# Kernel tuning notes

Hardware: AMD Instinct MI355X
Metric: run time of the kernel (lower is better)

## Reference

```python
import jax, jax.numpy as jnp
import numpy as np


def setup_inputs() -> dict:
    key = jax.random.key(0)
    k = jax.random.split(key, 6)
    B, N, Cin, Cd, nE = 64, 197, 768, 256, 8192
    return {
        "z": jax.random.normal(k[0], (B, N, Cin), dtype=jnp.float32),
        "emb": jax.random.truncated_normal(k[1], -3.0, 3.0, (nE, Cd), dtype=jnp.float32),
        "W_compress": jax.random.normal(k[2], (Cin, Cd), dtype=jnp.float32) * 0.02,
        "b_compress": jnp.zeros((Cd,), dtype=jnp.float32),
        "W_expand": jax.random.normal(k[3], (Cd, Cin), dtype=jnp.float32) * 0.02,
        "b_expand": jnp.zeros((Cin,), dtype=jnp.float32),
    }


def reference(z, emb, W_compress, b_compress, W_expand, b_expand):
    # compress: [B,N,Cin] -> [B,N,Cd]
    zc = jnp.einsum('bnc,cd->bnd', z, W_compress) + b_compress
    zf = zc.reshape(-1, zc.shape[-1])  # [M, Cd]
    # squared distances to codebook: ||z||^2 + ||e||^2 - 2 z.e  -> [M, nE]
    d = (jnp.sum(zf * zf, axis=1, keepdims=True)
         + jnp.sum(emb * emb, axis=1)
         - 2.0 * (zf @ emb.T))
    indices = jnp.argmin(d, axis=1)  # [M]
    z_q = emb[indices]               # gather [M, Cd]
    sg = jax.lax.stop_gradient
    # training-mode commitment/codebook loss
    loss = jnp.mean((sg(z_q) - zf) ** 2) + 2.0 * jnp.mean((z_q - sg(zf)) ** 2)
    # straight-through estimator
    z_q = sg(z_q) + zf - sg(zf)
    z_q = z_q.reshape(zc.shape)
    out = jnp.einsum('bnd,dc->bnc', z_q, W_expand) + b_expand  # [B,N,Cin]
    return (out, loss)
```

## Files before the change

### kernel.cpp

```cpp
#include <hip/hip_runtime.h>
#include <stdint.h>

#define M_TOK 12608
#define MPAD  12672
#define CIN   768
#define CD    256
#define NE    8192
#define NCHUNK 8
#define CHUNK  1024

typedef unsigned long long u64;
typedef unsigned int u32;
typedef _Float16 f16;
typedef _Float16 f16x8 __attribute__((ext_vector_type(8)));
typedef _Float16 f16x4 __attribute__((ext_vector_type(4)));
typedef float f32x4 __attribute__((ext_vector_type(4)));

#if __has_builtin(__builtin_amdgcn_global_load_lds)
#define HAVE_GLL 1
#else
#define HAVE_GLL 0
#endif

__device__ __forceinline__ void stage16(const f16* src, char* lds_base, int lane)
{
#if HAVE_GLL
    __builtin_amdgcn_global_load_lds(
        (__attribute__((address_space(1))) void*)(src),
        (__attribute__((address_space(3))) void*)(lds_base), 16, 0, 0);
#else
    *(f16x8*)(lds_base + lane * 16) = *(const f16x8*)src;
#endif
}

__global__ __launch_bounds__(256) void k_enorm(const float* __restrict__ emb,
                                               float* __restrict__ enorm,
                                               f16* __restrict__ embf16,
                                               float* __restrict__ loss_slot)
{
    if (blockIdx.x == 0 && threadIdx.x == 0) *loss_slot = 0.0f;
    int row  = blockIdx.x * 4 + (threadIdx.x >> 6);
    int lane = threadIdx.x & 63;
    float4 v = *(const float4*)&emb[(size_t)row * CD + lane * 4];
    f16x4 hv = { (f16)v.x, (f16)v.y, (f16)v.z, (f16)v.w };
    *(f16x4*)&embf16[(size_t)row * CD + lane * 4] = hv;
    float s = v.x*v.x + v.y*v.y + v.z*v.z + v.w*v.w;
    #pragma unroll
    for (int o = 32; o; o >>= 1) s += __shfl_down(s, o, 64);
    if (lane == 0) enorm[row] = s;
}

__global__ __launch_bounds__(256) void k_prep_w(const float* __restrict__ Wc,
                                                const float* __restrict__ We,
                                                f16* __restrict__ wchi,
                                                f16* __restrict__ wclo,
                                                f16* __restrict__ wet)
{
    int tid = blockIdx.x * 256 + threadIdx.x;
    {
        int n = tid & 255, k = tid >> 8;
        float v = Wc[(size_t)k * CD + n];
        f16 h = (f16)v;
        wchi[(size_t)n * CIN + k] = h;
        wclo[(size_t)n * CIN + k] = (f16)(v - (float)h);
    }
    {
        int d = tid / CIN, c = tid - d * CIN;
        wet[(size_t)c * CD + d] = (f16)We[(size_t)d * CIN + c];
    }
}

__global__ __launch_bounds__(256) void k_prep_z(const float* __restrict__ z,
                                                f16* __restrict__ zhi,
                                                f16* __restrict__ zlo)
{
    size_t i4 = (size_t)blockIdx.x * 256 + threadIdx.x;
    float4 v = ((const float4*)z)[i4];
    f16x4 h = { (f16)v.x, (f16)v.y, (f16)v.z, (f16)v.w };
    f16x4 lo = { (f16)(v.x - (float)h.x), (f16)(v.y - (float)h.y),
                 (f16)(v.z - (float)h.z), (f16)(v.w - (float)h.w) };
    ((f16x4*)zhi)[i4] = h;
    ((f16x4*)zlo)[i4] = lo;
}

__global__ __launch_bounds__(256) void k_init_zc(const float* __restrict__ bc,
                                                 float* __restrict__ zc)
{
    size_t i4 = (size_t)blockIdx.x * 256 + threadIdx.x;
    ((float4*)zc)[i4] = ((const float4*)bc)[i4 & 63];
}

__global__ __launch_bounds__(256) void k_zcfin(const float* __restrict__ zc,
                                               f16* __restrict__ zcf16)
{
    size_t i4 = (size_t)blockIdx.x * 256 + threadIdx.x;
    float4 v = ((const float4*)zc)[i4];
    f16x4 h = { (f16)v.x, (f16)v.y, (f16)v.z, (f16)v.w };
    ((f16x4*)zcf16)[i4] = h;
}

__global__ __launch_bounds__(256) void k_compress3(const f16* __restrict__ zhi,
                                                   const f16* __restrict__ zlo,
                                                   const f16* __restrict__ wchi,
                                                   const f16* __restrict__ wclo,
                                                   float* __restrict__ zc)
{
    __shared__ __align__(16) f16 As[128 * 64];
    __shared__ __align__(16) f16 Bs[128 * 64];

    const int t = threadIdx.x;
    const int w = t >> 6, l = t & 63;
    const int wrow = (w >> 1) * 64, wcol = (w & 1) * 64;
    const int m0   = blockIdx.x * 128;
    const int col0 = blockIdx.y * 128;
    const int term = blockIdx.z;

    const f16* A = (term < 2)  ? zhi  : zlo;
    const f16* B = (term == 1) ? wclo : wchi;

    const int cg   = (t & 7) ^ ((t >> 3) & 7);
    const int rloc = t >> 3;
    const f16* asrc[4]; const f16* bsrc[4];
    #pragma unroll
    for (int i = 0; i < 4; ++i) {
        int r = i * 32 + rloc;
        int am = m0 + r; am = am < M_TOK ? am : (M_TOK - 1);
        asrc[i] = A + (size_t)am * CIN + cg * 8;
        bsrc[i] = B + (size_t)(col0 + r) * CIN + cg * 8;
    }
    const int prd0 = (l >> 4) ^ (l & 7);
    const int prd1 = (4 + (l >> 4)) ^ (l & 7);

    f32x4 acc[4][4];
    #pragma unroll
    for (int a = 0; a < 4; ++a)
        #pragma unroll
        for (int b = 0; b < 4; ++b) acc[a][b] = (f32x4){0.f,0.f,0.f,0.f};

    for (int ks = 0; ks < CIN / 64; ++ks) {
        __syncthreads();
        #pragma unroll
        for (int i = 0; i < 4; ++i) {
            stage16(asrc[i] + ks * 64, (char*)As + (i * 256 + w * 64) * 16, l);
            stage16(bsrc[i] + ks * 64, (char*)Bs + (i * 256 + w * 64) * 16, l);
        }
        __syncthreads();
        #pragma unroll
        for (int kk = 0; kk < 2; ++kk) {
            const int pofs = (kk ? prd1 : prd0) * 16;
            f16x8 af[4], bf[4];
            #pragma unroll
            for (int tm = 0; tm < 4; ++tm)
                af[tm] = *(const f16x8*)((const char*)As + (wrow + tm*16 + (l & 15)) * 128 + pofs);
            #pragma unroll
            for (int tn = 0; tn < 4; ++tn)
                bf[tn] = *(const f16x8*)((const char*)Bs + (wcol + tn*16 + (l & 15)) * 128 + pofs);
            #pragma unroll
            for (int tm = 0; tm < 4; ++tm)
                #pragma unroll
                for (int tn = 0; tn < 4; ++tn)
                    acc[tm][tn] = __builtin_amdgcn_mfma_f32_16x16x32_f16(af[tm], bf[tn], acc[tm][tn], 0, 0, 0);
        }
    }

    #pragma unroll
    for (int tm = 0; tm < 4; ++tm) {
        #pragma unroll
        for (int reg = 0; reg < 4; ++reg) {
            int row = m0 + wrow + tm * 16 + (l >> 4) * 4 + reg;
            if (row < M_TOK) {
                #pragma unroll
                for (int tn = 0; tn < 4; ++tn) {
                    int col = col0 + wcol + tn * 16 + (l & 15);
                    unsafeAtomicAdd(&zc[(size_t)row * CD + col], acc[tm][tn][reg]);
                }
            }
        }
    }
}

__global__ __launch_bounds__(256) void k_dist_mfma(const f16* __restrict__ zcf16,
                                                   const f16* __restrict__ embf16,
                                                   const float* __restrict__ enorm,
                                                   u64* __restrict__ part)
{
    __shared__ __align__(16) f16 As[128 * 64];
    __shared__ __align__(16) f16 Bs[128 * 64];
    __shared__ u64 wred[128][2][2];

    const int t = threadIdx.x;
    const int w = t >> 6, l = t & 63;
    const int wrow = (w >> 1) * 64, wcol = (w & 1) * 64;
    const int m0    = blockIdx.x * 128;
    const int chunk = blockIdx.y;

    const int cg   = (t & 7) ^ ((t >> 3) & 7);
    const int rloc = t >> 3;
    const f16* asrc[4]; const f16* bsrc[4];
    #pragma unroll
    for (int i = 0; i < 4; ++i) {
        int r = i * 32 + rloc;
        int am = m0 + r; am = am < M_TOK ? am : (M_TOK - 1);
        asrc[i] = zcf16 + (size_t)am * CD + cg * 8;
        bsrc[i] = embf16 + (size_t)r * CD + cg * 8;
    }
    const int prd0 = (l >> 4) ^ (l & 7);
    const int prd1 = (4 + (l >> 4)) ^ (l & 7);

    float bd[16];
    int   bcol[16];
    #pragma unroll
    for (int s = 0; s < 16; ++s) { bd[s] = __builtin_inff(); bcol[s] = 0; }

    for (int tile = 0; tile < 8; ++tile) {
        const int j0 = chunk * CHUNK + tile * 128;
        f32x4 acc[4][4];
        #pragma unroll
        for (int a = 0; a < 4; ++a)
            #pragma unroll
            for (int b = 0; b < 4; ++b) acc[a][b] = (f32x4){0.f,0.f,0.f,0.f};

        for (int ks = 0; ks < 4; ++ks) {
            __syncthreads();
            #pragma unroll
            for (int i = 0; i < 4; ++i) {
                stage16(asrc[i] + ks * 64, (char*)As + (i * 256 + w * 64) * 16, l);
                stage16(bsrc[i] + (size_t)j0 * CD + ks * 64, (char*)Bs + (i * 256 + w * 64) * 16, l);
            }
            __syncthreads();
            #pragma unroll
            for (int kk = 0; kk < 2; ++kk) {
                const int pofs = (kk ? prd1 : prd0) * 16;
                f16x8 af[4], bf[4];
                #pragma unroll
                for (int tm = 0; tm < 4; ++tm)
                    af[tm] = *(const f16x8*)((const char*)As + (wrow + tm*16 + (l & 15)) * 128 + pofs);
                #pragma unroll
                for (int tn = 0; tn < 4; ++tn)
                    bf[tn] = *(const f16x8*)((const char*)Bs + (wcol + tn*16 + (l & 15)) * 128 + pofs);
                #pragma unroll
                for (int tm = 0; tm < 4; ++tm)
                    #pragma unroll
                    for (int tn = 0; tn < 4; ++tn)
                        acc[tm][tn] = __builtin_amdgcn_mfma_f32_16x16x32_f16(af[tm], bf[tn], acc[tm][tn], 0, 0, 0);
            }
        }

        const int cb = j0 + wcol + (l & 15);
        float en0 = enorm[cb], en1 = enorm[cb + 16], en2 = enorm[cb + 32], en3 = enorm[cb + 48];
        #pragma unroll
        for (int tm = 0; tm < 4; ++tm) {
            #pragma unroll
            for (int reg = 0; reg < 4; ++reg) {
                const int s = tm * 4 + reg;
                float d0 = fmaf(acc[tm][0][reg], -2.f, en0);
                float d1 = fmaf(acc[tm][1][reg], -2.f, en1);
                float d2 = fmaf(acc[tm][2][reg], -2.f, en2);
                float d3 = fmaf(acc[tm][3][reg], -2.f, en3);
                float da = d1 < d0 ? d1 : d0;  int ca = d1 < d0 ? cb + 16 : cb;
                float db = d3 < d2 ? d3 : d2;  int cc = d3 < d2 ? cb + 48 : cb + 32;
                float dm = db < da ? db : da;  int cm = db < da ? cc : ca;
                if (dm < bd[s]) { bd[s] = dm; bcol[s] = cm; }
            }
        }
    }

    #pragma unroll
    for (int tm = 0; tm < 4; ++tm) {
        #pragma unroll
        for (int reg = 0; reg < 4; ++reg) {
            const int s = tm * 4 + reg;
            u32 u = __float_as_uint(bd[s]);
            u = (u & 0x80000000u) ? ~u : (u | 0x80000000u);
            u64 b  = ((u64)u << 32) | (u32)bcol[s];
            u64 sc = ~0ull;
            #pragma unroll
            for (int off = 1; off <= 8; off <<= 1) {
                u64 ob = __shfl_xor(b, off, 64);
                u64 os = __shfl_xor(sc, off, 64);
                u64 nb = b < ob ? b : ob;
                u64 mx = b < ob ? ob : b;
                sc = sc < os ? sc : os;
                sc = sc < mx ? sc : mx;
                b = nb;
            }
            if ((l & 15) == 0) {
                int row = wrow + tm * 16 + (l >> 4) * 4 + reg;
                wred[row][w & 1][0] = b;
                wred[row][w & 1][1] = sc;
            }
        }
    }
    __syncthreads();
    if (t < 128) {
        u64 b0 = wred[t][0][0], s0 = wred[t][0][1];
        u64 b1 = wred[t][1][0], s1 = wred[t][1][1];
        u64 B  = b0 < b1 ? b0 : b1;
        u64 mx = b0 < b1 ? b1 : b0;
        u64 S  = s0 < s1 ? s0 : s1;
        S = S < mx ? S : mx;
        int row = m0 + t;
        if (row < M_TOK) {
            part[((size_t)row * NCHUNK + chunk) * 2 + 0] = B;
            part[((size_t)row * NCHUNK + chunk) * 2 + 1] = S;
        }
    }
}

__global__ __launch_bounds__(256) void k_rescore(const float* __restrict__ zc,
                                                 const float* __restrict__ emb,
                                                 const float* __restrict__ enorm,
                                                 const u64* __restrict__ part,
                                                 int* __restrict__ idxp,
                                                 float* __restrict__ loss_slot)
{
    const int row = blockIdx.x * 4 + (threadIdx.x >> 6);
    const int l   = threadIdx.x & 63;
    __shared__ float lsum[4];

    float4 zr = *(const float4*)&zc[(size_t)row * CD + l * 4];
    u64 best = ~0ull;
    for (int c = 0; c < 16; ++c) {
        u64 key = part[(size_t)row * 16 + c];
        int col = (int)((u32)key & (NE - 1));
        float4 er = *(const float4*)&emb[(size_t)col * CD + l * 4];
        float p = zr.x*er.x + zr.y*er.y + zr.z*er.z + zr.w*er.w;
        #pragma unroll
        for (int o = 32; o; o >>= 1) p += __shfl_xor(p, o, 64);
        float d = fmaf(p, -2.f, enorm[col]);
        u32 u = __float_as_uint(d);
        u = (u & 0x80000000u) ? ~u : (u | 0x80000000u);
        u64 k2 = ((u64)u << 32) | (u32)col;
        best = k2 < best ? k2 : best;
    }
    float zn = zr.x*zr.x + zr.y*zr.y + zr.z*zr.z + zr.w*zr.w;
    #pragma unroll
    for (int o = 32; o; o >>= 1) zn += __shfl_xor(zn, o, 64);

    u32 hi = (u32)(best >> 32);
    float dbest = (hi & 0x80000000u) ? __uint_as_float(hi & 0x7fffffffu)
                                     : __uint_as_float(~hi);
    if (l == 0) {
        idxp[row] = (int)((u32)best & (NE - 1));
        lsum[threadIdx.x >> 6] = dbest + zn;
    }
    __syncthreads();
    if (threadIdx.x == 0) {
        float tot = lsum[0] + lsum[1] + lsum[2] + lsum[3];
        atomicAdd(loss_slot, tot * (3.0f / 3227648.0f));
    }
}

__global__ __launch_bounds__(256) void k_expand_mfma(const f16* __restrict__ embf16,
                                                     const int* __restrict__ idxp,
                                                     const f16* __restrict__ wet,
                                                     const float* __restrict__ be,
                                                     float* __restrict__ out)
{
    __shared__ __align__(16) f16 As[128 * 64];
    __shared__ __align__(16) f16 Bs[128 * 64];

    const int t = threadIdx.x;
    const int w = t >> 6, l = t & 63;
    const int wrow = (w >> 1) * 64, wcol = (w & 1) * 64;
    const int m0   = blockIdx.x * 128;
    const int col0 = blockIdx.y * 128;

    const int cg   = (t & 7) ^ ((t >> 3) & 7);
    const int rloc = t >> 3;
    const f16* asrc[4]; const f16* bsrc[4];
    #pragma unroll
    for (int i = 0; i < 4; ++i) {
        int r = i * 32 + rloc;
        int m = m0 + r; m = m < M_TOK ? m : (M_TOK - 1);
        int er = idxp[m];
        asrc[i] = embf16 + (size_t)er * CD + cg * 8;
        bsrc[i] = wet + (size_t)(col0 + r) * CD + cg * 8;
    }
    const int prd0 = (l >> 4) ^ (l & 7);
    const int prd1 = (4 + (l >> 4)) ^ (l & 7);

    f32x4 acc[4][4];
    #pragma unroll
    for (int a = 0; a < 4; ++a)
        #pragma unroll
        for (int b = 0; b < 4; ++b) acc[a][b] = (f32x4){0.f,0.f,0.f,0.f};

    for (int ks = 0; ks < 4; ++ks) {
        __syncthreads();
        #pragma unroll
        for (int i = 0; i < 4; ++i) {
            stage16(asrc[i] + ks * 64, (char*)As + (i * 256 + w * 64) * 16, l);
            stage16(bsrc[i] + ks * 64, (char*)Bs + (i * 256 + w * 64) * 16, l);
        }
        __syncthreads();
        #pragma unroll
        for (int kk = 0; kk < 2; ++kk) {
            const int pofs = (kk ? prd1 : prd0) * 16;
            f16x8 af[4], bf[4];
            #pragma unroll
            for (int tm = 0; tm < 4; ++tm)
                af[tm] = *(const f16x8*)((const char*)As + (wrow + tm*16 + (l & 15)) * 128 + pofs);
            #pragma unroll
            for (int tn = 0; tn < 4; ++tn)
                bf[tn] = *(const f16x8*)((const char*)Bs + (wcol + tn*16 + (l & 15)) * 128 + pofs);
            #pragma unroll
            for (int tm = 0; tm < 4; ++tm)
                #pragma unroll
                for (int tn = 0; tn < 4; ++tn)
                    acc[tm][tn] = __builtin_amdgcn_mfma_f32_16x16x32_f16(af[tm], bf[tn], acc[tm][tn], 0, 0, 0);
        }
    }

    float bev[4];
    #pragma unroll
    for (int tn = 0; tn < 4; ++tn) bev[tn] = be[col0 + wcol + tn * 16 + (l & 15)];
    #pragma unroll
    for (int tm = 0; tm < 4; ++tm) {
        #pragma unroll
        for (int reg = 0; reg < 4; ++reg) {
            int row = m0 + wrow + tm * 16 + (l >> 4) * 4 + reg;
            if (row < M_TOK) {
                #pragma unroll
                for (int tn = 0; tn < 4; ++tn) {
                    int col = col0 + wcol + tn * 16 + (l & 15);
                    out[(size_t)row * CIN + col] = acc[tm][tn][reg] + bev[tn];
                }
            }
        }
    }
}

#define BK1 16
__global__ __launch_bounds__(256) void k_compress(const float* __restrict__ z,
                                                  const float* __restrict__ W,
                                                  const float* __restrict__ bias,
                                                  float* __restrict__ zc,
                                                  f16* __restrict__ zcf16)
{
    __shared__ __align__(16) float As[BK1][64 + 4];
    __shared__ __align__(16) float Bs[BK1][64 + 4];
    const int t  = threadIdx.x;
    const int tx = t & 15, ty = t >> 4;
    const int row0 = blockIdx.x * 64;
    const int col0 = blockIdx.y * 64;

    const int la_r = t >> 2;
    const int la_k = (t & 3) << 2;
    const int lb_k = t >> 4;
    const int lb_n = (t & 15) << 2;

    float acc[4][4] = {};

    for (int k0 = 0; k0 < CIN; k0 += BK1) {
        float4 a4 = *(const float4*)&z[(size_t)(row0 + la_r) * CIN + k0 + la_k];
        float4 b4 = *(const float4*)&W[(size_t)(k0 + lb_k) * CD + col0 + lb_n];
        __syncthreads();
        As[la_k + 0][la_r] = a4.x; As[la_k + 1][la_r] = a4.y;
        As[la_k + 2][la_r] = a4.z; As[la_k + 3][la_r] = a4.w;
        *(float4*)&Bs[lb_k][lb_n] = b4;
        __syncthreads();
        #pragma unroll
        for (int k = 0; k < BK1; ++k) {
            float a[4], b[4];
            *(float4*)&a[0] = *(const float4*)&As[k][ty * 4];
            *(float4*)&b[0] = *(const float4*)&Bs[k][tx * 4];
            #pragma unroll
            for (int i = 0; i < 4; ++i)
                #pragma unroll
                for (int j = 0; j < 4; ++j)
                    acc[i][j] = fmaf(a[i], b[j], acc[i][j]);
        }
    }

    float4 bb = *(const float4*)&bias[col0 + tx * 4];
    #pragma unroll
    for (int i = 0; i < 4; ++i) {
        float4 v;
        v.x = acc[i][0] + bb.x; v.y = acc[i][1] + bb.y;
        v.z = acc[i][2] + bb.z; v.w = acc[i][3] + bb.w;
        size_t off = (size_t)(row0 + ty * 4 + i) * CD + col0 + tx * 4;
        *(float4*)&zc[off] = v;
        f16x4 hv = { (f16)v.x, (f16)v.y, (f16)v.z, (f16)v.w };
        *(f16x4*)&zcf16[off] = hv;
    }
}

extern "C" void kernel_launch(void* const* d_in, const int* in_sizes, int n_in,
                              void* d_out, int out_size, void* d_ws, size_t ws_size,
                              hipStream_t stream)
{
    (void)in_sizes; (void)n_in; (void)out_size;

    const float* z   = (const float*)d_in[0];
    const float* emb = (const float*)d_in[1];
    const float* Wc  = (const float*)d_in[2];
    const float* bc  = (const float*)d_in[3];
    const float* We  = (const float*)d_in[4];
    const float* be  = (const float*)d_in[5];

    float* out       = (float*)d_out;
    float* loss_slot = out + (size_t)M_TOK * CIN;

    char* base = (char*)d_ws;
    size_t off = 0;
    auto align_up = [](size_t x) { return (x + 255) & ~(size_t)255; };

    float* enorm = (float*)(base + off); off = align_up(off + (size_t)NE * 4);
    u64*   part  = (u64*)(base + off);   off = align_up(off + (size_t)M_TOK * 16 * 8);
    int*   idxp  = (int*)(base + off);   off = align_up(off + (size_t)M_TOK * 4);
    f16*   embf16= (f16*)(base + off);   off = align_up(off + (size_t)NE * CD * 2);
    f16*   zcf16 = (f16*)(base + off);   off = align_up(off + (size_t)MPAD * CD * 2);
    f16*   wet   = (f16*)(base + off);   off = align_up(off + (size_t)CIN * CD * 2);
    f16*   wchi  = (f16*)(base + off);   off = align_up(off + (size_t)CD * CIN * 2);
    f16*   wclo  = (f16*)(base + off);   off = align_up(off + (size_t)CD * CIN * 2);

    const size_t zsplit_bytes = (size_t)M_TOK * CIN * 2;
    bool have_split = (ws_size >= off + 2 * zsplit_bytes);
    f16 *zhi = nullptr, *zlo = nullptr;
    if (have_split) {
        zhi = (f16*)(base + off); off = align_up(off + zsplit_bytes);
        zlo = (f16*)(base + off); off = align_up(off + zsplit_bytes);
    }
    const size_t zc_bytes = (size_t)M_TOK * CD * 4;
    float* zc = (ws_size >= off + zc_bytes) ? (float*)(base + off) : out;

    k_enorm <<<NE / 4, 256, 0, stream>>>(emb, enorm, embf16, loss_slot);
    k_prep_w<<<(CIN * CD) / 256, 256, 0, stream>>>(Wc, We, wchi, wclo, wet);

    if (have_split) {
        k_prep_z  <<<((size_t)M_TOK * CIN / 4) / 256, 256, 0, stream>>>(z, zhi, zlo);
        k_init_zc <<<((size_t)M_TOK * CD / 4) / 256, 256, 0, stream>>>(bc, zc);
        k_compress3<<<dim3(MPAD / 128, CD / 128, 3), 256, 0, stream>>>(zhi, zlo, wchi, wclo, zc);
        k_zcfin   <<<((size_t)M_TOK * CD / 4) / 256, 256, 0, stream>>>(zc, zcf16);
    } else {
        k_compress<<<dim3(M_TOK / 64, CD / 64), 256, 0, stream>>>(z, Wc, bc, zc, zcf16);
    }

    k_dist_mfma  <<<dim3(MPAD / 128, NCHUNK), 256, 0, stream>>>(zcf16, embf16, enorm, part);
    k_rescore    <<<M_TOK / 4, 256, 0, stream>>>(zc, emb, enorm, part, idxp, loss_slot);
    k_expand_mfma<<<dim3(MPAD / 128, CIN / 128), 256, 0, stream>>>(embf16, idxp, wet, be, out);
}
```

Measured before the change: 315.9 us.

## Fuse prep kernels, fuse split-f16 compress terms with bias, widen distance tiles

Merges the emb-norm, weight-prep and z-split kernels into one launch with block-range dispatch. The compress GEMM now computes all three hi/lo product terms inside one block and writes zc plus its f16 copy with the bias added directly. This removes the atomic adds, the zc init kernel and the finalize kernel. The distance kernel now processes 256 codebook columns per tile with 4x8 accumulators per wave and launch_bounds(256,2). That cuts A-tile restaging but raises register and LDS pressure.

```diff
diff --git a/kernel.cpp b/kernel.cpp
--- a/kernel.cpp
+++ b/kernel.cpp
@@ -33,234 +33,242 @@
 #endif
 }
 
-__global__ __launch_bounds__(256) void k_enorm(const float* __restrict__ emb,
-                                               float* __restrict__ enorm,
-                                               f16* __restrict__ embf16,
-                                               float* __restrict__ loss_slot)
-{
-    if (blockIdx.x == 0 && threadIdx.x == 0) *loss_slot = 0.0f;
-    int row  = blockIdx.x * 4 + (threadIdx.x >> 6);
-    int lane = threadIdx.x & 63;
-    float4 v = *(const float4*)&emb[(size_t)row * CD + lane * 4];
-    f16x4 hv = { (f16)v.x, (f16)v.y, (f16)v.z, (f16)v.w };
-    *(f16x4*)&embf16[(size_t)row * CD + lane * 4] = hv;
-    float s = v.x*v.x + v.y*v.y + v.z*v.z + v.w*v.w;
-    #pragma unroll
-    for (int o = 32; o; o >>= 1) s += __shfl_down(s, o, 64);
-    if (lane == 0) enorm[row] = s;
-}
-
-__global__ __launch_bounds__(256) void k_prep_w(const float* __restrict__ Wc,
-                                                const float* __restrict__ We,
-                                                f16* __restrict__ wchi,
-                                                f16* __restrict__ wclo,
-                                                f16* __restrict__ wet)
-{
-    int tid = blockIdx.x * 256 + threadIdx.x;
-    {
-        int n = tid & 255, k = tid >> 8;
-        float v = Wc[(size_t)k * CD + n];
-        f16 h = (f16)v;
-        wchi[(size_t)n * CIN + k] = h;
-        wclo[(size_t)n * CIN + k] = (f16)(v - (float)h);
-    }
-    {
-        int d = tid / CIN, c = tid - d * CIN;
-        wet[(size_t)c * CD + d] = (f16)We[(size_t)d * CIN + c];
-    }
-}
-
-__global__ __launch_bounds__(256) void k_prep_z(const float* __restrict__ z,
-                                                f16* __restrict__ zhi,
-                                                f16* __restrict__ zlo)
-{
-    size_t i4 = (size_t)blockIdx.x * 256 + threadIdx.x;
-    float4 v = ((const float4*)z)[i4];
-    f16x4 h = { (f16)v.x, (f16)v.y, (f16)v.z, (f16)v.w };
-    f16x4 lo = { (f16)(v.x - (float)h.x), (f16)(v.y - (float)h.y),
-                 (f16)(v.z - (float)h.z), (f16)(v.w - (float)h.w) };
-    ((f16x4*)zhi)[i4] = h;
-    ((f16x4*)zlo)[i4] = lo;
-}
-
-__global__ __launch_bounds__(256) void k_init_zc(const float* __restrict__ bc,
-                                                 float* __restrict__ zc)
-{
-    size_t i4 = (size_t)blockIdx.x * 256 + threadIdx.x;
-    ((float4*)zc)[i4] = ((const float4*)bc)[i4 & 63];
-}
-
-__global__ __launch_bounds__(256) void k_zcfin(const float* __restrict__ zc,
-                                               f16* __restrict__ zcf16)
-{
-    size_t i4 = (size_t)blockIdx.x * 256 + threadIdx.x;
-    float4 v = ((const float4*)zc)[i4];
-    f16x4 h = { (f16)v.x, (f16)v.y, (f16)v.z, (f16)v.w };
-    ((f16x4*)zcf16)[i4] = h;
-}
-
-__global__ __launch_bounds__(256) void k_compress3(const f16* __restrict__ zhi,
-                                                   const f16* __restrict__ zlo,
-                                                   const f16* __restrict__ wchi,
-                                                   const f16* __restrict__ wclo,
-                                                   float* __restrict__ zc)
-{
-    __shared__ __align__(16) f16 As[128 * 64];
-    __shared__ __align__(16) f16 Bs[128 * 64];
+__global__ __launch_bounds__(256) void k_prep(const float* __restrict__ emb,
+                                              const float* __restrict__ Wc,
+                                              const float* __restrict__ We,
+                                              const float* __restrict__ z,
+                                              float* __restrict__ enorm,
+                                              f16* __restrict__ embf16,
+                                              f16* __restrict__ wchi,
+                                              f16* __restrict__ wclo,
+                                              f16* __restrict__ wet,
+                                              f16* __restrict__ zhi,
+                                              f16* __restrict__ zlo,
+                                              float* __restrict__ loss_slot)
+{
+    const int b = blockIdx.x;
+    const int t = threadIdx.x;
+    if (b < 2048) {
+        if (b == 0 && t == 0) *loss_slot = 0.0f;
+        int row  = b * 4 + (t >> 6);
+        int lane = t & 63;
+        float4 v = *(const float4*)&emb[(size_t)row * CD + lane * 4];
+        f16x4 hv = { (f16)v.x, (f16)v.y, (f16)v.z, (f16)v.w };
+        *(f16x4*)&embf16[(size_t)row * CD + lane * 4] = hv;
+        float s = v.x*v.x + v.y*v.y + v.z*v.z + v.w*v.w;
+        #pragma unroll
+        for (int o = 32; o; o >>= 1) s += __shfl_down(s, o, 64);
+        if (lane == 0) enorm[row] = s;
+    } else if (b < 2048 + 768) {
+        int tid = (b - 2048) * 256 + t;
+        {
+            int n = tid & 255, k = tid >> 8;
+            float v = Wc[(size_t)k * CD + n];
+            f16 h = (f16)v;
+            wchi[(size_t)n * CIN + k] = h;
+            wclo[(size_t)n * CIN + k] = (f16)(v - (float)h);
+        }
+        {
+            int d = tid / CIN, c = tid - d * CIN;
+            wet[(size_t)c * CD + d] = (f16)We[(size_t)d * CIN + c];
+        }
+    } else {
+        size_t i4 = (size_t)(b - 2816) * 256 + t;
+        float4 v = ((const float4*)z)[i4];
+        f16x4 h = { (f16)v.x, (f16)v.y, (f16)v.z, (f16)v.w };
+        f16x4 lo = { (f16)(v.x - (float)h.x), (f16)(v.y - (float)h.y),
+                     (f16)(v.z - (float)h.z), (f16)(v.w - (float)h.w) };
+        ((f16x4*)zhi)[i4] = h;
+        ((f16x4*)zlo)[i4] = lo;
+    }
+}
+
+__global__ __launch_bounds__(256) void k_compress_f(const f16* __restrict__ zhi,
+                                                    const f16* __restrict__ zlo,
+                                                    const f16* __restrict__ wchi,
+                                                    const f16* __restrict__ wclo,
+                                                    const float* __restrict__ bc,
+                                                    float* __restrict__ zc,
+                                                    f16* __restrict__ zcf16)
+{
+    __shared__ __align__(16) f16 Ah[128 * 64];
+    __shared__ __align__(16) f16 Al[128 * 64];
+    __shared__ __align__(16) f16 Bh[64 * 64];
+    __shared__ __align__(16) f16 Bl[64 * 64];
 
     const int t = threadIdx.x;
     const int w = t >> 6, l = t & 63;
-    const int wrow = (w >> 1) * 64, wcol = (w & 1) * 64;
+    const int wrow = w * 32;
     const int m0   = blockIdx.x * 128;
-    const int col0 = blockIdx.y * 128;
-    const int term = blockIdx.z;
-
-    const f16* A = (term < 2)  ? zhi  : zlo;
-    const f16* B = (term == 1) ? wclo : wchi;
+    const int col0 = blockIdx.y * 64;
 
     const int cg   = (t & 7) ^ ((t >> 3) & 7);
     const int rloc = t >> 3;
-    const f16* asrc[4]; const f16* bsrc[4];
+    const f16* ahsrc[4]; const f16* alsrc[4];
     #pragma unroll
     for (int i = 0; i < 4; ++i) {
-        int r = i * 32 + rloc;
-        int am = m0 + r; am = am < M_TOK ? am : (M_TOK - 1);
-        asrc[i] = A + (size_t)am * CIN + cg * 8;
-        bsrc[i] = B + (size_t)(col0 + r) * CIN + cg * 8;
-    }
-    const int prd0 = (l >> 4) ^ (l & 7);
-    const int prd1 = (4 + (l >> 4)) ^ (l & 7);
-
-    f32x4 acc[4][4];
-    #pragma unroll
-    for (int a = 0; a < 4; ++a)
-        #pragma unroll
-        for (int b = 0; b < 4; ++b) acc[a][b] = (f32x4){0.f,0.f,0.f,0.f};
+        int am = m0 + i * 32 + rloc; am = am < M_TOK ? am : (M_TOK - 1);
+        ahsrc[i] = zhi + (size_t)am * CIN + cg * 8;
+        alsrc[i] = zlo + (size_t)am * CIN + cg * 8;
+    }
+    const f16* bhsrc[2]; const f16* blsrc[2];
+    #pragma unroll
+    for (int i = 0; i < 2; ++i) {
+        int br = col0 + i * 32 + rloc;
+        bhsrc[i] = wchi + (size_t)br * CIN + cg * 8;
+        blsrc[i] = wclo + (size_t)br * CIN + cg * 8;
+    }
+
+    f32x4 acc[2][4];
+    #pragma unroll
+    for (int a = 0; a < 2; ++a)
+        #pragma unroll
+        for (int b2 = 0; b2 < 4; ++b2) acc[a][b2] = (f32x4){0.f,0.f,0.f,0.f};
 
     for (int ks = 0; ks < CIN / 64; ++ks) {
         __syncthreads();
         #pragma unroll
         for (int i = 0; i < 4; ++i) {
-            stage16(asrc[i] + ks * 64, (char*)As + (i * 256 + w * 64) * 16, l);
-            stage16(bsrc[i] + ks * 64, (char*)Bs + (i * 256 + w * 64) * 16, l);
+            stage16(ahsrc[i] + ks * 64, (char*)Ah + (i * 256 + w * 64) * 16, l);
+            stage16(alsrc[i] + ks * 64, (char*)Al + (i * 256 + w * 64) * 16, l);
+        }
+        #pragma unroll
+        for (int i = 0; i < 2; ++i) {
+            stage16(bhsrc[i] + ks * 64, (char*)Bh + (i * 256 + w * 64) * 16, l);
+            stage16(blsrc[i] + ks * 64, (char*)Bl + (i * 256 + w * 64) * 16, l);
         }
         __syncthreads();
         #pragma unroll
         for (int kk = 0; kk < 2; ++kk) {
-            const int pofs = (kk ? prd1 : prd0) * 16;
-            f16x8 af[4], bf[4];
-            #pragma unroll
-            for (int tm = 0; tm < 4; ++tm)
-                af[tm] = *(const f16x8*)((const char*)As + (wrow + tm*16 + (l & 15)) * 128 + pofs);
-            #pragma unroll
-            for (int tn = 0; tn < 4; ++tn)
-                bf[tn] = *(const f16x8*)((const char*)Bs + (wcol + tn*16 + (l & 15)) * 128 + pofs);
-            #pragma unroll
-            for (int tm = 0; tm < 4; ++tm)
-                #pragma unroll
-                for (int tn = 0; tn < 4; ++tn)
-                    acc[tm][tn] = __builtin_amdgcn_mfma_f32_16x16x32_f16(af[tm], bf[tn], acc[tm][tn], 0, 0, 0);
-        }
-    }
-
-    #pragma unroll
-    for (int tm = 0; tm < 4; ++tm) {
+            const int pofs = ((kk * 4 + (l >> 4)) ^ (l & 7)) * 16;
+            f16x8 ah[2], al[2], bh[4], bl[4];
+            #pragma unroll
+            for (int tm = 0; tm < 2; ++tm) {
+                ah[tm] = *(const f16x8*)((const char*)Ah + (wrow + tm*16 + (l & 15)) * 128 + pofs);
+                al[tm] = *(const f16x8*)((const char*)Al + (wrow + tm*16 + (l & 15)) * 128 + pofs);
+            }
+            #pragma unroll
+            for (int tn = 0; tn < 4; ++tn) {
+                bh[tn] = *(const f16x8*)((const char*)Bh + (tn*16 + (l & 15)) * 128 + pofs);
+                bl[tn] = *(const f16x8*)((const char*)Bl + (tn*16 + (l & 15)) * 128 + pofs);
+            }
+            #pragma unroll
+            for (int tm = 0; tm < 2; ++tm)
+                #pragma unroll
+                for (int tn = 0; tn < 4; ++tn) {
+                    f32x4 a = acc[tm][tn];
+                    a = __builtin_amdgcn_mfma_f32_16x16x32_f16(ah[tm], bh[tn], a, 0, 0, 0);
+                    a = __builtin_amdgcn_mfma_f32_16x16x32_f16(ah[tm], bl[tn], a, 0, 0, 0);
+                    a = __builtin_amdgcn_mfma_f32_16x16x32_f16(al[tm], bh[tn], a, 0, 0, 0);
+                    acc[tm][tn] = a;
+                }
+        }
+    }
+
+    #pragma unroll
+    for (int tm = 0; tm < 2; ++tm) {
         #pragma unroll
         for (int reg = 0; reg < 4; ++reg) {
             int row = m0 + wrow + tm * 16 + (l >> 4) * 4 + reg;
             if (row < M_TOK) {
                 #pragma unroll
                 for (int tn = 0; tn < 4; ++tn) {
-                    int col = col0 + wcol + tn * 16 + (l & 15);
-                    unsafeAtomicAdd(&zc[(size_t)row * CD + col], acc[tm][tn][reg]);
+                    int col = col0 + tn * 16 + (l & 15);
+                    float v = acc[tm][tn][reg] + bc[col];
+                    zc[(size_t)row * CD + col] = v;
+                    zcf16[(size_t)row * CD + col] = (f16)v;
                 }
             }
         }
     }
 }
 
-__global__ __launch_bounds__(256) void k_dist_mfma(const f16* __restrict__ zcf16,
-                                                   const f16* __restrict__ embf16,
-                                                   const float* __restrict__ enorm,
-                                                   u64* __restrict__ part)
+__global__ __launch_bounds__(256, 2) void k_dist_mfma(const f16* __restrict__ zcf16,
+                                                      const f16* __restrict__ embf16,
+                                                      const float* __restrict__ enorm,
+                                                      u64* __restrict__ part)
 {
     __shared__ __align__(16) f16 As[128 * 64];
-    __shared__ __align__(16) f16 Bs[128 * 64];
+    __shared__ __align__(16) f16 Bs[256 * 64];
     __shared__ u64 wred[128][2][2];
 
     const int t = threadIdx.x;
     const int w = t >> 6, l = t & 63;
-    const int wrow = (w >> 1) * 64, wcol = (w & 1) * 64;
+    const int wrow  = (w >> 1) * 64;
+    const int wcolh = (w & 1);
     const int m0    = blockIdx.x * 128;
     const int chunk = blockIdx.y;
 
     const int cg   = (t & 7) ^ ((t >> 3) & 7);
     const int rloc = t >> 3;
-    const f16* asrc[4]; const f16* bsrc[4];
+    const f16* asrc[4];
     #pragma unroll
     for (int i = 0; i < 4; ++i) {
-        int r = i * 32 + rloc;
-        int am = m0 + r; am = am < M_TOK ? am : (M_TOK - 1);
+        int am = m0 + i * 32 + rloc; am = am < M_TOK ? am : (M_TOK - 1);
         asrc[i] = zcf16 + (size_t)am * CD + cg * 8;
-        bsrc[i] = embf16 + (size_t)r * CD + cg * 8;
-    }
-    const int prd0 = (l >> 4) ^ (l & 7);
-    const int prd1 = (4 + (l >> 4)) ^ (l & 7);
+    }
 
     float bd[16];
     int   bcol[16];
     #pragma unroll
     for (int s = 0; s < 16; ++s) { bd[s] = __builtin_inff(); bcol[s] = 0; }
 
-    for (int tile = 0; tile < 8; ++tile) {
-        const int j0 = chunk * CHUNK + tile * 128;
-        f32x4 acc[4][4];
+    for (int jp = 0; jp < 4; ++jp) {
+        const int j0 = chunk * CHUNK + jp * 256;
+        const f16* bbase = embf16 + (size_t)(j0 + rloc) * CD + cg * 8;
+
+        f32x4 acc[4][8];
         #pragma unroll
         for (int a = 0; a < 4; ++a)
             #pragma unroll
-            for (int b = 0; b < 4; ++b) acc[a][b] = (f32x4){0.f,0.f,0.f,0.f};
+            for (int b2 = 0; b2 < 8; ++b2) acc[a][b2] = (f32x4){0.f,0.f,0.f,0.f};
 
         for (int ks = 0; ks < 4; ++ks) {
             __syncthreads();
             #pragma unroll
-            for (int i = 0; i < 4; ++i) {
+            for (int i = 0; i < 4; ++i)
                 stage16(asrc[i] + ks * 64, (char*)As + (i * 256 + w * 64) * 16, l);
-                stage16(bsrc[i] + (size_t)j0 * CD + ks * 64, (char*)Bs + (i * 256 + w * 64) * 16, l);
-            }
+            #pragma unroll
+            for (int i = 0; i < 8; ++i)
+                stage16(bbase + (size_t)i * 32 * CD + ks * 64,
+                        (char*)Bs + (i * 256 + w * 64) * 16, l);
             __syncthreads();
             #pragma unroll
             for (int kk = 0; kk < 2; ++kk) {
-                const int pofs = (kk ? prd1 : prd0) * 16;
-                f16x8 af[4], bf[4];
+                const int pofs = ((kk * 4 + (l >> 4)) ^ (l & 7)) * 16;
+                f16x8 af[4], bf[8];
                 #pragma unroll
                 for (int tm = 0; tm < 4; ++tm)
                     af[tm] = *(const f16x8*)((const char*)As + (wrow + tm*16 + (l & 15)) * 128 + pofs);
                 #pragma unroll
-                for (int tn = 0; tn < 4; ++tn)
-                    bf[tn] = *(const f16x8*)((const char*)Bs + (wcol + tn*16 + (l & 15)) * 128 + pofs);
+                for (int tn = 0; tn < 8; ++tn)
+                    bf[tn] = *(const f16x8*)((const char*)Bs + (wcolh*128 + tn*16 + (l & 15)) * 128 + pofs);
                 #pragma unroll
                 for (int tm = 0; tm < 4; ++tm)
                     #pragma unroll
-                    for (int tn = 0; tn < 4; ++tn)
+                    for (int tn = 0; tn < 8; ++tn)
                         acc[tm][tn] = __builtin_amdgcn_mfma_f32_16x16x32_f16(af[tm], bf[tn], acc[tm][tn], 0, 0, 0);
             }
         }
 
-        const int cb = j0 + wcol + (l & 15);
-        float en0 = enorm[cb], en1 = enorm[cb + 16], en2 = enorm[cb + 32], en3 = enorm[cb + 48];
+        const int cb = j0 + wcolh * 128 + (l & 15);
+        float en[8];
+        #pragma unroll
+        for (int tn = 0; tn < 8; ++tn) en[tn] = enorm[cb + tn * 16];
         #pragma unroll
         for (int tm = 0; tm < 4; ++tm) {
             #pragma unroll
             for (int reg = 0; reg < 4; ++reg) {
                 const int s = tm * 4 + reg;
-                float d0 = fmaf(acc[tm][0][reg], -2.f, en0);
-                float d1 = fmaf(acc[tm][1][reg], -2.f, en1);
-                float d2 = fmaf(acc[tm][2][reg], -2.f, en2);
-                float d3 = fmaf(acc[tm][3][reg], -2.f, en3);
-                float da = d1 < d0 ? d1 : d0;  int ca = d1 < d0 ? cb + 16 : cb;
-                float db = d3 < d2 ? d3 : d2;  int cc = d3 < d2 ? cb + 48 : cb + 32;
-                float dm = db < da ? db : da;  int cm = db < da ? cc : ca;
-                if (dm < bd[s]) { bd[s] = dm; bcol[s] = cm; }
+                float dm = bd[s]; int cm = bcol[s];
+                #pragma unroll
+                for (int tn = 0; tn < 8; ++tn) {
+                    float d = fmaf(acc[tm][tn][reg], -2.f, en[tn]);
+                    bool lt = d < dm;
+                    dm = lt ? d : dm;
+                    cm = lt ? cb + tn * 16 : cm;
+                }
+                bd[s] = dm; bcol[s] = cm;
             }
         }
     }
@@ -525,15 +533,14 @@
     const size_t zc_bytes = (size_t)M_TOK * CD * 4;
     float* zc = (ws_size >= off + zc_bytes) ? (float*)(base + off) : out;
 
-    k_enorm <<<NE / 4, 256, 0, stream>>>(emb, enorm, embf16, loss_slot);
-    k_prep_w<<<(CIN * CD) / 256, 256, 0, stream>>>(Wc, We, wchi, wclo, wet);
-
     if (have_split) {
-        k_prep_z  <<<((size_t)M_TOK * CIN / 4) / 256, 256, 0, stream>>>(z, zhi, zlo);
-        k_init_zc <<<((size_t)M_TOK * CD / 4) / 256, 256, 0, stream>>>(bc, zc);
-        k_compress3<<<dim3(MPAD / 128, CD / 128, 3), 256, 0, stream>>>(zhi, zlo, wchi, wclo, zc);
-        k_zcfin   <<<((size_t)M_TOK * CD / 4) / 256, 256, 0, stream>>>(zc, zcf16);
+        k_prep      <<<12272, 256, 0, stream>>>(emb, Wc, We, z, enorm, embf16,
+                                                wchi, wclo, wet, zhi, zlo, loss_slot);
+        k_compress_f<<<dim3(MPAD / 128, CD / 64), 256, 0, stream>>>(zhi, zlo, wchi, wclo,
+                                                                    bc, zc, zcf16);
     } else {
+        k_prep    <<<2816, 256, 0, stream>>>(emb, Wc, We, z, enorm, embf16,
+                                             wchi, wclo, wet, (f16*)wchi, (f16*)wclo, loss_slot);
         k_compress<<<dim3(M_TOK / 64, CD / 64), 256, 0, stream>>>(z, Wc, bc, zc, zcf16);
     }
 
```

After: 324.2 us. 1.03x slower.
